# Optimization experiments

Measured on AMD Instinct MI355X. Metric: run time of the kernel, lower is better.

## Reference

```python
import jax, jax.numpy as jnp
import numpy as np

C_IN = 512


def _rms(h, gamma):
    # F.normalize(x, dim=1) * sqrt(C) * gamma  (channel_first, h: [b, c, l])
    c = h.shape[1]
    n = jnp.sqrt(jnp.sum(h * h, axis=1, keepdims=True))
    return h / jnp.maximum(n, 1e-12) * (c ** 0.5) * gamma[None, :, None]


def _pw(w, b, h):
    # 1x1 conv == pointwise linear over channel dim; h: [b, c, l]
    return jnp.einsum('oc,bcl->bol', w, h) + b[None, :, None]


def setup_inputs() -> dict:
    key = jax.random.key(0)
    ks = jax.random.split(key, 10)
    B, C, T, H, W = 1, C_IN, 16, 32, 32
    inp = {'x': jax.random.normal(ks[0], (B, C, T, H, W), jnp.float32)}
    names = ['qs', 'ks', 'vs', 'ps', 'qt', 'kt', 'vt', 'pt']
    for i, n in enumerate(names):
        inp[n + '_w'] = jax.random.normal(ks[i + 1], (C, C), jnp.float32) * 0.02
        inp[n + '_b'] = jnp.zeros((C,), jnp.float32)
    inp['norm_s_gamma'] = jnp.ones((C,), jnp.float32)
    inp['norm_t_gamma'] = jnp.ones((C,), jnp.float32)
    inp['max_temporal_window'] = 8
    return inp


def reference(x, qs_w, qs_b, ks_w, ks_b, vs_w, vs_b, ps_w, ps_b,
              qt_w, qt_b, kt_w, kt_b, vt_w, vt_b, pt_w, pt_b,
              norm_s_gamma, norm_t_gamma, max_temporal_window):
    B, C, T, H, W = x.shape
    scale = C ** -0.5

    # ---- spatial attention: (b t) c (h w) ----
    xs = x.transpose(0, 2, 1, 3, 4).reshape(B * T, C, H * W)
    h = _rms(xs, norm_s_gamma)
    q = _pw(qs_w, qs_b, h)
    k = _pw(ks_w, ks_b, h)
    v = _pw(vs_w, vs_b, h)
    scores = jnp.einsum('bcl,bcm->blm', q, k) * scale  # [bt, HW, HW]
    attn = jax.nn.softmax(scores, axis=-1)
    o = jnp.einsum('bcm,blm->bcl', v, attn)
    xs = xs + _pw(ps_w, ps_b, o)
    x = xs.reshape(B, T, C, H, W).transpose(0, 2, 1, 3, 4)

    # ---- temporal attention: (b h w) c t, causal + bounded window ----
    xt = x.transpose(0, 3, 4, 1, 2).reshape(B * H * W, C, T)
    h = _rms(xt, norm_t_gamma)
    q = _pw(qt_w, qt_b, h)
    k = _pw(kt_w, kt_b, h)
    v = _pw(vt_w, vt_b, h)
    scores = jnp.einsum('bcl,bcm->blm', q, k) * scale  # [bhw, T, T]
    i = jnp.arange(T)[:, None]
    j = jnp.arange(T)[None, :]
    allowed = j <= i  # causal
    if max_temporal_window is not None and max_temporal_window > 0:
        allowed = allowed & (i - j < max_temporal_window)  # sliding window
    mask = jnp.where(allowed, 0.0, jnp.finfo(scores.dtype).min)
    attn = jax.nn.softmax(scores + mask[None], axis=-1)
    o = jnp.einsum('bcm,blm->bcl', v, attn)
    xt = xt + _pw(pt_w, pt_b, o)
    x = xt.reshape(B, H, W, C, T).transpose(0, 3, 4, 1, 2)
    return x
```

## Files before the change

kernel.cpp:

```cpp
#include <hip/hip_runtime.h>

typedef __attribute__((ext_vector_type(8))) short bf16x8;
typedef __attribute__((ext_vector_type(4))) float f32x4;

__device__ __forceinline__ short f2bf(float f) {
  union { float f; unsigned u; } a; a.f = f;
  unsigned r = a.u + 0x7fffu + ((a.u >> 16) & 1u);
  return (short)(r >> 16);
}
__device__ __forceinline__ float bf2f(short s) {
  union { unsigned u; float f; } a;
  a.u = ((unsigned)(unsigned short)s) << 16; return a.f;
}
__device__ __forceinline__ float blo(unsigned u) { union { unsigned u; float f; } a; a.u = u << 16; return a.f; }
__device__ __forceinline__ float bhi(unsigned u) { union { unsigned u; float f; } a; a.u = u & 0xffff0000u; return a.f; }
__device__ __forceinline__ unsigned packbf(float lo, float hi) {
  return (unsigned)(unsigned short)f2bf(lo) | ((unsigned)(unsigned short)f2bf(hi) << 16);
}
__device__ __forceinline__ void ldscp16(const void* g, void* l) {
  __builtin_amdgcn_global_load_lds((const __attribute__((address_space(1))) void*)g,
                                   (__attribute__((address_space(3))) void*)l, 16, 0, 0);
}
__device__ __forceinline__ void stv(float* p, float v) { *p = v; }
__device__ __forceinline__ void stv(short* p, float v) { *p = f2bf(v); }

__global__ __launch_bounds__(256) void zero_f(float* __restrict__ p) {
  p[blockIdx.x * 256 + threadIdx.x] = 0.f;
}

__global__ __launch_bounds__(256) void cvt_w(
    const float* __restrict__ w0, const float* __restrict__ w1,
    const float* __restrict__ w2, const float* __restrict__ w3,
    const float* __restrict__ w4, const float* __restrict__ w5,
    const float* __restrict__ w6, const float* __restrict__ w7,
    const float* __restrict__ g_s, const float* __restrict__ g_t,
    short* __restrict__ out) {
  int idx = blockIdx.x * 256 + threadIdx.x;
  const float* ws[8] = {w0, w1, w2, w3, w4, w5, w6, w7};
  int wi = idx >> 18, c = idx & 511;
  float g = 1.f;
  if (wi <= 2) g = g_s[c];
  else if (wi >= 4 && wi <= 6) g = g_t[c];
  out[idx] = f2bf(ws[wi][idx & 262143] * g);
}

__global__ __launch_bounds__(256) void cvt_b(
    const float* __restrict__ b0, const float* __restrict__ b1,
    const float* __restrict__ b2, const float* __restrict__ b3,
    const float* __restrict__ b4, const float* __restrict__ b5,
    const float* __restrict__ b6, const float* __restrict__ b7,
    float* __restrict__ out) {
  int idx = blockIdx.x * 256 + threadIdx.x;
  const float* bs[8] = {b0, b1, b2, b3, b4, b5, b6, b7};
  out[idx] = bs[idx >> 9][idx & 511];
}

__global__ __launch_bounds__(256) void txp_sumsq(
    const float* __restrict__ src, short* __restrict__ dst,
    float* __restrict__ ss) {
  constexpr long N = 16384;
  __shared__ short T[64][66];
  __shared__ float part[16][16][4];
  const int tid = threadIdx.x;
  const long n0 = (long)blockIdx.x * 64;
  const int c0 = blockIdx.y * 64;
  const int n4 = (tid & 15) * 4;
  float s0 = 0.f, s1 = 0.f, s2 = 0.f, s3 = 0.f;
#pragma unroll
  for (int i = 0; i < 4; ++i) {
    int cl = i * 16 + (tid >> 4);
    float4 v = *(const float4*)&src[(long)(c0 + cl) * N + n0 + n4];
    s0 += v.x * v.x; s1 += v.y * v.y; s2 += v.z * v.z; s3 += v.w * v.w;
    T[n4 + 0][cl] = f2bf(v.x); T[n4 + 1][cl] = f2bf(v.y);
    T[n4 + 2][cl] = f2bf(v.z); T[n4 + 3][cl] = f2bf(v.w);
  }
  part[tid >> 4][tid & 15][0] = s0; part[tid >> 4][tid & 15][1] = s1;
  part[tid >> 4][tid & 15][2] = s2; part[tid >> 4][tid & 15][3] = s3;
  __syncthreads();
  if (tid < 64) {
    float s = 0.f;
#pragma unroll
    for (int cg = 0; cg < 16; ++cg) s += part[cg][tid >> 2][tid & 3];
    atomicAdd(&ss[n0 + tid], s);
  }
#pragma unroll
  for (int p = 0; p < 4; ++p) {
    int nl = p * 16 + (tid >> 4);
    int cl = (tid & 15) * 4;
    uint2 o;
    o.x = (unsigned)(unsigned short)T[nl][cl] |
          ((unsigned)(unsigned short)T[nl][cl + 1] << 16);
    o.y = (unsigned)(unsigned short)T[nl][cl + 2] |
          ((unsigned)(unsigned short)T[nl][cl + 3] << 16);
    *(uint2*)&dst[(n0 + nl) * 512 + c0 + cl] = o;
  }
}

template <typename OutT, int BIAS_MODE, int SCALE_MODE, bool RESID, bool EXP>
__global__ __launch_bounds__(256, 3) void gemm_nt(
    const short* __restrict__ A, const short* __restrict__ B,
    OutT* __restrict__ D, const float* __restrict__ bias,
    const float* __restrict__ ssv, float* __restrict__ rs,
    const float* __restrict__ resid,
    int K, int lda, int ldb, int ldd,
    long aBatch, long bBatch, long dBatch, long sBatch, float scale) {
  __shared__ short As[128 * 64];
  __shared__ short Bs[128 * 64];
  const int tid = threadIdx.x;
  const int bz = blockIdx.z;
  const long i0 = (long)blockIdx.x * 128;
  const long j0 = (long)blockIdx.y * 128;
  const short* Ab = A + bz * aBatch + i0 * lda;
  const short* Bb = B + bz * bBatch + j0 * ldb;
  const int srow = tid >> 3, scol = tid & 7;
  const int lane = tid & 63;
  const int wr = ((tid >> 7) & 1) * 64;
  const int wc = ((tid >> 6) & 1) * 64;
  const int quad = lane >> 4, l15 = lane & 15;

  f32x4 acc[4][4] = {};

  for (int k0 = 0; k0 < K; k0 += 64) {
    __syncthreads();
#pragma unroll
    for (int p = 0; p < 4; ++p) {
      int row = p * 32 + srow;
      int gc = (scol ^ (row & 7)) << 3;
      ldscp16(Ab + (long)row * lda + k0 + gc, &As[p * 2048 + tid * 8]);
    }
#pragma unroll
    for (int p = 0; p < 4; ++p) {
      int row = p * 32 + srow;
      int gc = (scol ^ (row & 7)) << 3;
      ldscp16(Bb + (long)row * ldb + k0 + gc, &Bs[p * 2048 + tid * 8]);
    }
    __syncthreads();
#pragma unroll
    for (int kk = 0; kk < 2; ++kk) {
      bf16x8 af[4], bfr[4];
#pragma unroll
      for (int a = 0; a < 4; ++a) {
        int row = wr + a * 16 + l15;
        int g = kk * 4 + quad;
        af[a] = *(const bf16x8*)&As[row * 64 + ((g ^ (row & 7)) << 3)];
      }
#pragma unroll
      for (int b = 0; b < 4; ++b) {
        int row = wc + b * 16 + l15;
        int g = kk * 4 + quad;
        bfr[b] = *(const bf16x8*)&Bs[row * 64 + ((g ^ (row & 7)) << 3)];
      }
#pragma unroll
      for (int a = 0; a < 4; ++a)
#pragma unroll
        for (int b = 0; b < 4; ++b)
          acc[a][b] = __builtin_amdgcn_mfma_f32_16x16x32_bf16(af[a], bfr[b], acc[a][b], 0, 0, 0);
    }
  }

  const long Doff = bz * dBatch;
#pragma unroll
  for (int a = 0; a < 4; ++a) {
    const int rb = (int)i0 + wr + a * 16 + quad * 4;
    float rsc[4];
    if (SCALE_MODE == 1) {
#pragma unroll
      for (int r = 0; r < 4; ++r)
        rsc[r] = 22.627416997969522f / fmaxf(sqrtf(ssv[rb + r]), 1e-12f);
    }
    if (SCALE_MODE == 3) {
#pragma unroll
      for (int r = 0; r < 4; ++r)
        rsc[r] = 1.f / ssv[bz * sBatch + rb + r];
    }
    float rowpart[4] = {0.f, 0.f, 0.f, 0.f};
#pragma unroll
    for (int b = 0; b < 4; ++b) {
      const int cc = (int)j0 + wc + b * 16 + l15;
      float csc = 1.f;
      if (SCALE_MODE == 2)
        csc = 22.627416997969522f / fmaxf(sqrtf(ssv[cc]), 1e-12f);
#pragma unroll
      for (int r = 0; r < 4; ++r) {
        float val = acc[a][b][r] * scale;
        if (EXP) { val = __expf(val); rowpart[r] += val; }
        if (SCALE_MODE == 1 || SCALE_MODE == 3) val *= rsc[r];
        if (SCALE_MODE == 2) val *= csc;
        if (BIAS_MODE == 1) val += bias[rb + r];
        if (BIAS_MODE == 2) val += bias[cc];
        const long off = Doff + (long)(rb + r) * ldd + cc;
        if (RESID) val += resid[off];
        stv(D + off, val);
      }
    }
    if (EXP) {
#pragma unroll
      for (int r = 0; r < 4; ++r) {
        float s = rowpart[r];
#pragma unroll
        for (int off = 1; off < 16; off <<= 1) s += __shfl_xor(s, off);
        if (l15 == 0) atomicAdd(&rs[bz * sBatch + rb + r], s);
      }
    }
  }
}

__global__ __launch_bounds__(256) void temporal_attn_v3(
    const short* __restrict__ qkv, const int* __restrict__ wndp,
    short* __restrict__ o, float scale) {
  constexpr int RS = 1032;
  __shared__ short qk[16 * RS];
  __shared__ float Plds[16][17];
  const int tid = threadIdx.x;
  const int w = tid >> 6, lane = tid & 63;
  const int hw = blockIdx.x;
  const int wnd = *wndp;

#pragma unroll
  for (int i = 0; i < 8; ++i) {
    int ci = w * 8 + i;
    int t = ci >> 1, half = ci & 1;
    ldscp16(qkv + (long)(t * 1024 + hw) * 1536 + half * 512 + lane * 8,
            &qk[t * RS + half * 512 + lane * 8]);
  }
  const int c0 = lane * 8;
  uint4 vch[16];
#pragma unroll
  for (int tp = 0; tp < 16; ++tp)
    vch[tp] = *(const uint4*)(qkv + (long)(tp * 1024 + hw) * 1536 + 1024 + c0);
  __syncthreads();

  if (w == 0) {
    const int quad = lane >> 4, m = lane & 15;
    const short* rowp = &qk[m * RS + quad * 8];
    f32x4 sacc = {};
#pragma unroll
    for (int s = 0; s < 16; ++s) {
      bf16x8 aq = *(const bf16x8*)(rowp + s * 32);
      bf16x8 bk = *(const bf16x8*)(rowp + 512 + s * 32);
      sacc = __builtin_amdgcn_mfma_f32_16x16x32_bf16(aq, bk, sacc, 0, 0, 0);
    }
#pragma unroll
    for (int r = 0; r < 4; ++r) {
      const int i = quad * 4 + r;
      const int j = m;
      const bool allowed = (j <= i) && (wnd <= 0 || (i - j) < wnd);
      float val = allowed ? sacc[r] * scale : -1e30f;
      float mx = val;
#pragma unroll
      for (int off = 1; off < 16; off <<= 1) mx = fmaxf(mx, __shfl_xor(mx, off));
      float e = allowed ? __expf(val - mx) : 0.f;
      float sum = e;
#pragma unroll
      for (int off = 1; off < 16; off <<= 1) sum += __shfl_xor(sum, off);
      Plds[i][j] = e / sum;
    }
  }
  __syncthreads();

#pragma unroll
  for (int r = 0; r < 4; ++r) {
    const int t = w * 4 + r;
    const int tlo = (wnd > 0 && t - wnd + 1 > 0) ? t - wnd + 1 : 0;
    float a0 = 0.f, a1 = 0.f, a2 = 0.f, a3 = 0.f,
          a4 = 0.f, a5 = 0.f, a6 = 0.f, a7 = 0.f;
#pragma unroll
    for (int tp = 0; tp < 16; ++tp) {
      const float p = (tp >= tlo && tp <= t) ? Plds[t][tp] : 0.f;
      const uint4 vv = vch[tp];
      a0 += p * blo(vv.x); a1 += p * bhi(vv.x);
      a2 += p * blo(vv.y); a3 += p * bhi(vv.y);
      a4 += p * blo(vv.z); a5 += p * bhi(vv.z);
      a6 += p * blo(vv.w); a7 += p * bhi(vv.w);
    }
    uint4 ov;
    ov.x = packbf(a0, a1); ov.y = packbf(a2, a3);
    ov.z = packbf(a4, a5); ov.w = packbf(a6, a7);
    *(uint4*)(o + (long)(t * 1024 + hw) * 512 + c0) = ov;
  }
}

extern "C" void kernel_launch(void* const* d_in, const int* in_sizes, int n_in,
                              void* d_out, int out_size, void* d_ws, size_t ws_size,
                              hipStream_t stream) {
  const float* x    = (const float*)d_in[0];
  const float* qs_w = (const float*)d_in[1];
  const float* qs_b = (const float*)d_in[2];
  const float* ks_w = (const float*)d_in[3];
  const float* ks_b = (const float*)d_in[4];
  const float* vs_w = (const float*)d_in[5];
  const float* vs_b = (const float*)d_in[6];
  const float* ps_w = (const float*)d_in[7];
  const float* ps_b = (const float*)d_in[8];
  const float* qt_w = (const float*)d_in[9];
  const float* qt_b = (const float*)d_in[10];
  const float* kt_w = (const float*)d_in[11];
  const float* kt_b = (const float*)d_in[12];
  const float* vt_w = (const float*)d_in[13];
  const float* vt_b = (const float*)d_in[14];
  const float* pt_w = (const float*)d_in[15];
  const float* pt_b = (const float*)d_in[16];
  const float* g_s  = (const float*)d_in[17];
  const float* g_t  = (const float*)d_in[18];
  const int*   wnd  = (const int*)d_in[19];
  float* out = (float*)d_out;

  char* w = (char*)d_ws;
  short* Wb   = (short*)(w);
  float* Ball = (float*)(w + (4L << 20));
  float* ss_s = (float*)(w + (4L << 20) + (64 << 10));
  float* ss_t = (float*)(w + (4L << 20) + (128 << 10));
  float* rsum = (float*)(w + (4L << 20) + (192 << 10));
  short* hb   = (short*)(w + (5L << 20));
  short* QK   = (short*)(w + (21L << 20));
  short* vB   = (short*)(w + (53L << 20));
  short* oT   = (short*)(w + (69L << 20));
  short* S    = (short*)(w + (85L << 20));
  (void)in_sizes; (void)n_in; (void)out_size; (void)ws_size;

  const float scale = 0.04419417382415922f;

  zero_f<<<192, 256, 0, stream>>>(ss_s);
  cvt_w<<<8192, 256, 0, stream>>>(qs_w, ks_w, vs_w, ps_w, qt_w, kt_w, vt_w, pt_w,
                                  g_s, g_t, Wb);
  cvt_b<<<16, 256, 0, stream>>>(qs_b, ks_b, vs_b, ps_b, qt_b, kt_b, vt_b, pt_b, Ball);

  txp_sumsq<<<dim3(256, 8, 1), 256, 0, stream>>>(x, hb, ss_s);
  gemm_nt<short, 2, 1, false, false><<<dim3(128, 8, 1), 256, 0, stream>>>(
      hb, Wb, QK, Ball, ss_s, nullptr, nullptr, 512, 512, 512, 1024,
      0, 0, 0, 0, 1.f);
  gemm_nt<short, 1, 2, false, false><<<dim3(4, 128, 1), 256, 0, stream>>>(
      Wb + 2 * 262144, hb, vB, Ball + 1024, ss_s, nullptr, nullptr,
      512, 512, 512, 16384, 0, 0, 0, 0, 1.f);
  gemm_nt<short, 0, 0, false, true><<<dim3(8, 8, 16), 256, 0, stream>>>(
      QK, QK + 512, S, nullptr, nullptr, rsum, nullptr, 512, 1024, 1024, 1024,
      1024L * 1024, 1024L * 1024, 1024L * 1024, 1024, scale);
  gemm_nt<short, 0, 3, false, false><<<dim3(8, 4, 16), 256, 0, stream>>>(
      S, vB, oT, nullptr, rsum, nullptr, nullptr, 1024, 1024, 16384, 512,
      1024L * 1024, 1024L, 1024L * 512, 1024, 1.f);
  gemm_nt<float, 1, 0, true, false><<<dim3(4, 128, 1), 256, 0, stream>>>(
      Wb + 3 * 262144, oT, out, Ball + 1536, nullptr, nullptr, x,
      512, 512, 512, 16384, 0, 0, 0, 0, 1.f);

  txp_sumsq<<<dim3(256, 8, 1), 256, 0, stream>>>(out, hb, ss_t);
  gemm_nt<short, 2, 1, false, false><<<dim3(128, 12, 1), 256, 0, stream>>>(
      hb, Wb + 4 * 262144, QK, Ball + 2048, ss_t, nullptr, nullptr,
      512, 512, 512, 1536, 0, 0, 0, 0, 1.f);
  temporal_attn_v3<<<1024, 256, 0, stream>>>(QK, wnd, oT, scale);
  gemm_nt<float, 1, 0, true, false><<<dim3(4, 128, 1), 256, 0, stream>>>(
      Wb + 7 * 262144, oT, out, Ball + 3584, nullptr, nullptr, out,
      512, 512, 512, 16384, 0, 0, 0, 0, 1.f);
}
```

Before: 332.9 us.

## Fold V projection into output projection weights for both attentions

Precomputes Wp·Wv (with gamma folded) and a combined bias Wp·bv+bp, so attention is applied directly to bf16 raw input instead of a separately projected V. Spatial path drops the V GEMM and applies the RMS scale per key column in the score GEMM; temporal path drops V from the QKV GEMM and applies the RMS factor to the softmax weights. This removes one 16384x512x512 GEMM per stage at the cost of an extra bf16 copy of x and small weight-product kernels. Rounding differs because the fused weight is formed in bf16.

```diff
diff --git a/kernel.cpp b/kernel.cpp
--- a/kernel.cpp
+++ b/kernel.cpp
@@ -37,11 +37,17 @@
     short* __restrict__ out) {
   int idx = blockIdx.x * 256 + threadIdx.x;
   const float* ws[8] = {w0, w1, w2, w3, w4, w5, w6, w7};
-  int wi = idx >> 18, c = idx & 511;
-  float g = 1.f;
-  if (wi <= 2) g = g_s[c];
-  else if (wi >= 4 && wi <= 6) g = g_t[c];
-  out[idx] = f2bf(ws[wi][idx & 262143] * g);
+  int wi = idx >> 18, loc = idx & 262143;
+  int r = loc >> 9, q = loc & 511;
+  float v, g;
+  if (wi == 2 || wi == 6) {
+    v = ws[wi][q * 512 + r];
+    g = (wi == 2) ? g_s[r] : g_t[r];
+  } else {
+    v = ws[wi][loc];
+    g = (wi <= 1) ? g_s[q] : (wi == 4 || wi == 5) ? g_t[q] : 1.f;
+  }
+  out[idx] = f2bf(v * g);
 }
 
 __global__ __launch_bounds__(256) void cvt_b(
@@ -55,9 +61,30 @@
   out[idx] = bs[idx >> 9][idx & 511];
 }
 
+__global__ __launch_bounds__(64) void bias_fold(
+    const float* __restrict__ ps_w, const float* __restrict__ vs_b,
+    const float* __restrict__ ps_b, const float* __restrict__ pt_w,
+    const float* __restrict__ vt_b, const float* __restrict__ pt_b,
+    float* __restrict__ bt_s, float* __restrict__ bt_t) {
+  const int b = blockIdx.x, lane = threadIdx.x;
+  const bool sp = b < 512;
+  const float* W = sp ? ps_w : pt_w;
+  const float* vb = sp ? vs_b : vt_b;
+  const float* pb = sp ? ps_b : pt_b;
+  float* o = sp ? bt_s : bt_t;
+  const int r = b & 511;
+  float s = 0.f;
+#pragma unroll
+  for (int c = lane; c < 512; c += 64) s += W[r * 512 + c] * vb[c];
+#pragma unroll
+  for (int off = 32; off > 0; off >>= 1) s += __shfl_xor(s, off);
+  if (lane == 0) o[r] = s + pb[r];
+}
+
+template <bool WXB>
 __global__ __launch_bounds__(256) void txp_sumsq(
     const float* __restrict__ src, short* __restrict__ dst,
-    float* __restrict__ ss) {
+    short* __restrict__ xb, float* __restrict__ ss) {
   constexpr long N = 16384;
   __shared__ short T[64][66];
   __shared__ float part[16][16][4];
@@ -71,8 +98,15 @@
     int cl = i * 16 + (tid >> 4);
     float4 v = *(const float4*)&src[(long)(c0 + cl) * N + n0 + n4];
     s0 += v.x * v.x; s1 += v.y * v.y; s2 += v.z * v.z; s3 += v.w * v.w;
-    T[n4 + 0][cl] = f2bf(v.x); T[n4 + 1][cl] = f2bf(v.y);
-    T[n4 + 2][cl] = f2bf(v.z); T[n4 + 3][cl] = f2bf(v.w);
+    short b0 = f2bf(v.x), b1 = f2bf(v.y), b2 = f2bf(v.z), b3 = f2bf(v.w);
+    T[n4 + 0][cl] = b0; T[n4 + 1][cl] = b1;
+    T[n4 + 2][cl] = b2; T[n4 + 3][cl] = b3;
+    if (WXB) {
+      uint2 o;
+      o.x = (unsigned)(unsigned short)b0 | ((unsigned)(unsigned short)b1 << 16);
+      o.y = (unsigned)(unsigned short)b2 | ((unsigned)(unsigned short)b3 << 16);
+      *(uint2*)&xb[(long)(c0 + cl) * N + n0 + n4] = o;
+    }
   }
   part[tid >> 4][tid & 15][0] = s0; part[tid >> 4][tid & 15][1] = s1;
   part[tid >> 4][tid & 15][2] = s2; part[tid >> 4][tid & 15][3] = s3;
@@ -166,7 +200,8 @@
     if (SCALE_MODE == 1) {
 #pragma unroll
       for (int r = 0; r < 4; ++r)
-        rsc[r] = 22.627416997969522f / fmaxf(sqrtf(ssv[rb + r]), 1e-12f);
+        rsc[r] = 22.627416997969522f /
+                 fmaxf(sqrtf(ssv[bz * sBatch + rb + r]), 1e-12f);
     }
     if (SCALE_MODE == 3) {
 #pragma unroll
@@ -179,7 +214,8 @@
       const int cc = (int)j0 + wc + b * 16 + l15;
       float csc = 1.f;
       if (SCALE_MODE == 2)
-        csc = 22.627416997969522f / fmaxf(sqrtf(ssv[cc]), 1e-12f);
+        csc = 22.627416997969522f /
+              fmaxf(sqrtf(ssv[bz * sBatch + cc]), 1e-12f);
 #pragma unroll
       for (int r = 0; r < 4; ++r) {
         float val = acc[a][b][r] * scale;
@@ -205,11 +241,12 @@
   }
 }
 
-__global__ __launch_bounds__(256) void temporal_attn_v3(
-    const short* __restrict__ qkv, const int* __restrict__ wndp,
+__global__ __launch_bounds__(256) void temporal_attn_v4(
+    const short* __restrict__ qk, const short* __restrict__ hb,
+    const float* __restrict__ ss, const int* __restrict__ wndp,
     short* __restrict__ o, float scale) {
   constexpr int RS = 1032;
-  __shared__ short qk[16 * RS];
+  __shared__ short qs[16 * RS];
   __shared__ float Plds[16][17];
   const int tid = threadIdx.x;
   const int w = tid >> 6, lane = tid & 63;
@@ -220,19 +257,19 @@
   for (int i = 0; i < 8; ++i) {
     int ci = w * 8 + i;
     int t = ci >> 1, half = ci & 1;
-    ldscp16(qkv + (long)(t * 1024 + hw) * 1536 + half * 512 + lane * 8,
-            &qk[t * RS + half * 512 + lane * 8]);
+    ldscp16(qk + (long)(t * 1024 + hw) * 1024 + half * 512 + lane * 8,
+            &qs[t * RS + half * 512 + lane * 8]);
   }
   const int c0 = lane * 8;
   uint4 vch[16];
 #pragma unroll
   for (int tp = 0; tp < 16; ++tp)
-    vch[tp] = *(const uint4*)(qkv + (long)(tp * 1024 + hw) * 1536 + 1024 + c0);
+    vch[tp] = *(const uint4*)(hb + (long)(tp * 1024 + hw) * 512 + c0);
   __syncthreads();
 
   if (w == 0) {
     const int quad = lane >> 4, m = lane & 15;
-    const short* rowp = &qk[m * RS + quad * 8];
+    const short* rowp = &qs[m * RS + quad * 8];
     f32x4 sacc = {};
 #pragma unroll
     for (int s = 0; s < 16; ++s) {
@@ -240,6 +277,8 @@
       bf16x8 bk = *(const bf16x8*)(rowp + 512 + s * 32);
       sacc = __builtin_amdgcn_mfma_f32_16x16x32_bf16(aq, bk, sacc, 0, 0, 0);
     }
+    const float rmsm = 22.627416997969522f /
+                       fmaxf(sqrtf(ss[m * 1024 + hw]), 1e-12f);
 #pragma unroll
     for (int r = 0; r < 4; ++r) {
       const int i = quad * 4 + r;
@@ -253,7 +292,7 @@
       float sum = e;
 #pragma unroll
       for (int off = 1; off < 16; off <<= 1) sum += __shfl_xor(sum, off);
-      Plds[i][j] = e / sum;
+      Plds[i][j] = (e / sum) * rmsm;
     }
   }
   __syncthreads();
@@ -311,11 +350,14 @@
   float* ss_s = (float*)(w + (4L << 20) + (64 << 10));
   float* ss_t = (float*)(w + (4L << 20) + (128 << 10));
   float* rsum = (float*)(w + (4L << 20) + (192 << 10));
-  short* hb   = (short*)(w + (5L << 20));
-  short* QK   = (short*)(w + (21L << 20));
-  short* vB   = (short*)(w + (53L << 20));
-  short* oT   = (short*)(w + (69L << 20));
-  short* S    = (short*)(w + (85L << 20));
+  float* bt_s = (float*)(w + (4L << 20) + (256 << 10));
+  float* bt_t = (float*)(w + (4L << 20) + (260 << 10));
+  short* Wpv  = (short*)(w + (4L << 20) + (512 << 10));
+  short* hb   = (short*)(w + (6L << 20));
+  short* QK   = (short*)(w + (22L << 20));
+  short* xb   = (short*)(w + (54L << 20));
+  short* oT   = (short*)(w + (70L << 20));
+  short* S    = (short*)(w + (86L << 20));
   (void)in_sizes; (void)n_in; (void)out_size; (void)ws_size;
 
   const float scale = 0.04419417382415922f;
@@ -324,30 +366,31 @@
   cvt_w<<<8192, 256, 0, stream>>>(qs_w, ks_w, vs_w, ps_w, qt_w, kt_w, vt_w, pt_w,
                                   g_s, g_t, Wb);
   cvt_b<<<16, 256, 0, stream>>>(qs_b, ks_b, vs_b, ps_b, qt_b, kt_b, vt_b, pt_b, Ball);
-
-  txp_sumsq<<<dim3(256, 8, 1), 256, 0, stream>>>(x, hb, ss_s);
+  bias_fold<<<1024, 64, 0, stream>>>(ps_w, vs_b, ps_b, pt_w, vt_b, pt_b, bt_s, bt_t);
+  gemm_nt<short, 0, 0, false, false><<<dim3(4, 4, 2), 256, 0, stream>>>(
+      Wb + 3 * 262144, Wb + 2 * 262144, Wpv, nullptr, nullptr, nullptr, nullptr,
+      512, 512, 512, 512, 4 * 262144L, 4 * 262144L, 262144L, 0, 1.f);
+
+  txp_sumsq<true><<<dim3(256, 8, 1), 256, 0, stream>>>(x, hb, xb, ss_s);
   gemm_nt<short, 2, 1, false, false><<<dim3(128, 8, 1), 256, 0, stream>>>(
       hb, Wb, QK, Ball, ss_s, nullptr, nullptr, 512, 512, 512, 1024,
       0, 0, 0, 0, 1.f);
-  gemm_nt<short, 1, 2, false, false><<<dim3(4, 128, 1), 256, 0, stream>>>(
-      Wb + 2 * 262144, hb, vB, Ball + 1024, ss_s, nullptr, nullptr,
-      512, 512, 512, 16384, 0, 0, 0, 0, 1.f);
-  gemm_nt<short, 0, 0, false, true><<<dim3(8, 8, 16), 256, 0, stream>>>(
-      QK, QK + 512, S, nullptr, nullptr, rsum, nullptr, 512, 1024, 1024, 1024,
+  gemm_nt<short, 0, 2, false, true><<<dim3(8, 8, 16), 256, 0, stream>>>(
+      QK, QK + 512, S, nullptr, ss_s, rsum, nullptr, 512, 1024, 1024, 1024,
       1024L * 1024, 1024L * 1024, 1024L * 1024, 1024, scale);
   gemm_nt<short, 0, 3, false, false><<<dim3(8, 4, 16), 256, 0, stream>>>(
-      S, vB, oT, nullptr, rsum, nullptr, nullptr, 1024, 1024, 16384, 512,
+      S, xb, oT, nullptr, rsum, nullptr, nullptr, 1024, 1024, 16384, 512,
       1024L * 1024, 1024L, 1024L * 512, 1024, 1.f);
   gemm_nt<float, 1, 0, true, false><<<dim3(4, 128, 1), 256, 0, stream>>>(
-      Wb + 3 * 262144, oT, out, Ball + 1536, nullptr, nullptr, x,
-      512, 512, 512, 16384, 0, 0, 0, 0, 1.f);
-
-  txp_sumsq<<<dim3(256, 8, 1), 256, 0, stream>>>(out, hb, ss_t);
-  gemm_nt<short, 2, 1, false, false><<<dim3(128, 12, 1), 256, 0, stream>>>(
+      Wpv, oT, out, bt_s, nullptr, nullptr, x, 512, 512, 512, 16384,
+      0, 0, 0, 0, 1.f);
+
+  txp_sumsq<false><<<dim3(256, 8, 1), 256, 0, stream>>>(out, hb, nullptr, ss_t);
+  gemm_nt<short, 2, 1, false, false><<<dim3(128, 8, 1), 256, 0, stream>>>(
       hb, Wb + 4 * 262144, QK, Ball + 2048, ss_t, nullptr, nullptr,
-      512, 512, 512, 1536, 0, 0, 0, 0, 1.f);
-  temporal_attn_v3<<<1024, 256, 0, stream>>>(QK, wnd, oT, scale);
+      512, 512, 512, 1024, 0, 0, 0, 0, 1.f);
+  temporal_attn_v4<<<1024, 256, 0, stream>>>(QK, hb, ss_t, wnd, oT, scale);
   gemm_nt<float, 1, 0, true, false><<<dim3(4, 128, 1), 256, 0, stream>>>(
-      Wb + 7 * 262144, oT, out, Ball + 3584, nullptr, nullptr, out,
-      512, 512, 512, 16384, 0, 0, 0, 0, 1.f);
-}
+      Wpv + 262144, oT, out, bt_t, nullptr, nullptr, out, 512, 512, 512, 16384,
+      0, 0, 0, 0, 1.f);
+}
```

Measured after the change: 331.5 us. Within noise of the previous version (-0.4%).
